# Kernel tuning notes

Hardware: AMD Instinct MI355X
Metric: run time of the kernel (lower is better)

Reference implementation:

```python
import jax, jax.numpy as jnp
import numpy as np

D_MODEL = 1024
N_HEADS = 16
HEAD_DIM = D_MODEL // N_HEADS


def setup_inputs() -> dict:
    key = jax.random.key(0)
    k1, k2, k3 = jax.random.split(key, 3)
    x = jax.random.normal(k1, (4, 2048, D_MODEL), dtype=jnp.float32)
    # torch Linear(d, 3d, bias=False): y = x @ W.T ; store transposed weight [d, 3d]
    scale = 1.0 / np.sqrt(D_MODEL)
    W_qkv = jax.random.normal(k2, (D_MODEL, 3 * D_MODEL), dtype=jnp.float32) * scale
    W_proj = jax.random.normal(k3, (D_MODEL, D_MODEL), dtype=jnp.float32) * scale
    return {"x": x, "W_qkv": W_qkv, "W_proj": W_proj}


def reference(x, W_qkv, W_proj):
    B, T, C = x.shape
    h, d = N_HEADS, HEAD_DIM
    qkv = x @ W_qkv                      # [B,T,3C]
    q, k, v = jnp.split(qkv, 3, axis=-1)
    def split_heads(t):
        return t.reshape(B, T, h, d).transpose(0, 2, 1, 3)  # [B,h,T,d]
    q, k, v = map(split_heads, (q, k, v))
    att = jnp.einsum('bhqd,bhkd->bhqk', q, k) / np.sqrt(d)  # [B,h,T,T]
    causal = jnp.tril(jnp.ones((T, T), dtype=bool))
    att = jnp.where(causal, att, -jnp.inf)
    att = jax.nn.softmax(att, axis=-1)
    # dropout = 0.0 (eval mode): no-op
    y = jnp.einsum('bhqk,bhkd->bhqd', att, v)               # [B,h,T,d]
    y = y.transpose(0, 2, 1, 3).reshape(B, T, C)
    return y @ W_proj
```

## Files before the change

### kernel.cpp

```cpp
#include <hip/hip_runtime.h>

#define T_SEQ 2048
#define D_MODEL 1024
#define NB 4
#define NH 16
#define HD 64

typedef __attribute__((ext_vector_type(8))) __bf16 bf16x8;
typedef __attribute__((ext_vector_type(4))) __bf16 bf16x4;
typedef __attribute__((ext_vector_type(4))) float f32x4;

__device__ __forceinline__ void gload_lds16(const void* g, void* l) {
  __builtin_amdgcn_global_load_lds((const __attribute__((address_space(1))) unsigned int*)g,
                                   (__attribute__((address_space(3))) unsigned int*)l,
                                   16, 0, 0);
}

__device__ __forceinline__ unsigned int pack_bf16_2(float e0, float e1) {
  unsigned short u0 = __builtin_bit_cast(unsigned short, (__bf16)e0);
  unsigned short u1 = __builtin_bit_cast(unsigned short, (__bf16)e1);
  return (unsigned int)u0 | ((unsigned int)u1 << 16);
}

__global__ __launch_bounds__(256) void cvt_bf16_kernel(const float* __restrict__ s,
                                                       __bf16* __restrict__ d, int n) {
  int i = (blockIdx.x * 256 + threadIdx.x) * 8;
  if (i >= n) return;
  float4 a = *(const float4*)(s + i);
  float4 b = *(const float4*)(s + i + 4);
  bf16x8 v;
  v[0] = (__bf16)a.x; v[1] = (__bf16)a.y; v[2] = (__bf16)a.z; v[3] = (__bf16)a.w;
  v[4] = (__bf16)b.x; v[5] = (__bf16)b.y; v[6] = (__bf16)b.z; v[7] = (__bf16)b.w;
  *(bf16x8*)(d + i) = v;
}

__global__ __launch_bounds__(256) void transpose_cvt_kernel(const float* __restrict__ W,
                                                            __bf16* __restrict__ Wt,
                                                            int K, int N) {
  __shared__ float t[32][33];
  int tx = threadIdx.x, ty = threadIdx.y;
  int n0 = blockIdx.x * 32, k0 = blockIdx.y * 32;
#pragma unroll
  for (int r = 0; r < 4; ++r)
    t[ty + r * 8][tx] = W[(size_t)(k0 + ty + r * 8) * N + n0 + tx];
  __syncthreads();
#pragma unroll
  for (int r = 0; r < 4; ++r)
    Wt[(size_t)(n0 + ty + r * 8) * K + k0 + tx] = (__bf16)t[tx][ty + r * 8];
}

__global__ __launch_bounds__(256) void extract_vt_kernel(const __bf16* __restrict__ qkv,
                                                         __bf16* __restrict__ Vt) {
  __shared__ __bf16 t[32][34];
  int tx = threadIdx.x, ty = threadIdx.y;
  int tt = blockIdx.x * 32;
  int dt = blockIdx.y * 32;
  int bh = blockIdx.z;
  int b = bh >> 4, h = bh & 15;
#pragma unroll
  for (int r = 0; r < 4; ++r)
    t[ty + r * 8][tx] = qkv[(size_t)(b * T_SEQ + tt + ty + r * 8) * 3072 + 2048 + h * HD + dt + tx];
  __syncthreads();
#pragma unroll
  for (int r = 0; r < 4; ++r)
    Vt[(size_t)(bh * HD + dt + ty + r * 8) * T_SEQ + tt + tx] = t[tx][ty + r * 8];
}

template <typename OutT>
__global__ __launch_bounds__(256) void gemm_bt(const __bf16* __restrict__ A,
                                               const __bf16* __restrict__ Bt,
                                               OutT* __restrict__ C,
                                               int M, int N, int K) {
  __shared__ __bf16 lA[128 * 64];
  __shared__ __bf16 lB[128 * 64];
  int tid = threadIdx.x;
  int lane = tid & 63, w = tid >> 6;
  int wm = w >> 1, wn = w & 1;
  int bn = blockIdx.x, bm = blockIdx.y;
  f32x4 acc[4][4] = {};
  for (int kt = 0; kt < K; kt += 64) {
#pragma unroll
    for (int it = 0; it < 4; ++it) {
      int o = it * 4096 + tid * 16;
      int row = o >> 7;
      int ss = ((o >> 4) & 7) ^ (row & 7);
      gload_lds16(A + (size_t)(bm * 128 + row) * K + kt + ss * 8, (char*)lA + o);
      gload_lds16(Bt + (size_t)(bn * 128 + row) * K + kt + ss * 8, (char*)lB + o);
    }
    __syncthreads();
    bf16x8 af[4][2], bfv[4][2];
#pragma unroll
    for (int i = 0; i < 4; ++i)
#pragma unroll
      for (int kk = 0; kk < 2; ++kk) {
        int ra = wm * 64 + i * 16 + (lane & 15);
        int sa = ((lane >> 4) + kk * 4) ^ (ra & 7);
        af[i][kk] = *(const bf16x8*)((const char*)lA + ra * 128 + sa * 16);
        int rb = wn * 64 + i * 16 + (lane & 15);
        int sb = ((lane >> 4) + kk * 4) ^ (rb & 7);
        bfv[i][kk] = *(const bf16x8*)((const char*)lB + rb * 128 + sb * 16);
      }
#pragma unroll
    for (int kk = 0; kk < 2; ++kk)
#pragma unroll
      for (int i = 0; i < 4; ++i)
#pragma unroll
        for (int j = 0; j < 4; ++j)
          acc[i][j] = __builtin_amdgcn_mfma_f32_16x16x32_bf16(af[i][kk], bfv[j][kk], acc[i][j], 0, 0, 0);
    __syncthreads();
  }
#pragma unroll
  for (int i = 0; i < 4; ++i)
#pragma unroll
    for (int j = 0; j < 4; ++j)
#pragma unroll
      for (int r = 0; r < 4; ++r) {
        int row = bm * 128 + wm * 64 + i * 16 + (lane >> 4) * 4 + r;
        int col = bn * 128 + wn * 64 + j * 16 + (lane & 15);
        C[(size_t)row * N + col] = (OutT)acc[i][j][r];
      }
}

__global__ __launch_bounds__(256) void attn_kernel(const __bf16* __restrict__ qkv,
                                                   const __bf16* __restrict__ Vt,
                                                   __bf16* __restrict__ Y) {
  __shared__ __bf16 lK[2][64 * 64];
  __shared__ __bf16 lV[2][64 * 64];
  int tid = threadIdx.x, lane = tid & 63, w = tid >> 6;
  int q = lane & 15, g = lane >> 4;

  int l = blockIdx.x;
  int j0 = l >> 3;
  int pair = ((l & 7) << 3) | (j0 >> 4);
  int p = j0 & 15;
  int h = pair & 15;
  int b = pair >> 4;

  const float SCALE = 0.125f * 1.44269504088896f;
  const f32x4 fzero = {0.f, 0.f, 0.f, 0.f};

#pragma unroll 1
  for (int pass = 0; pass < 2; ++pass) {
    int qt = pass ? p : 31 - p;

    const __bf16* qp = qkv + (size_t)(b * T_SEQ + qt * 64 + w * 16 + q) * 3072 + h * HD;
    bf16x8 qf[2];
    qf[0] = *(const bf16x8*)(qp + g * 8);
    qf[1] = *(const bf16x8*)(qp + 32 + g * 8);
#pragma unroll
    for (int kk = 0; kk < 2; ++kk)
#pragma unroll
      for (int jj = 0; jj < 8; ++jj) qf[kk][jj] = (__bf16)((float)qf[kk][jj] * SCALE);

    float m = -INFINITY, lsum = 0.f;
    f32x4 yacc[4];
#pragma unroll
    for (int f = 0; f < 4; ++f) yacc[f] = fzero;

    asm volatile("s_waitcnt vmcnt(0)" ::: "memory");
    __builtin_amdgcn_sched_barrier(0);

    auto STAGE = [&](int kvt, int bi) {
#pragma unroll
      for (int it = 0; it < 2; ++it) {
        int o = it * 4096 + tid * 16;
        int row = o >> 7;
        int ss = ((o >> 4) & 7) ^ (row & 7);
        gload_lds16(qkv + (size_t)(b * T_SEQ + kvt * 64 + row) * 3072 + 1024 + h * HD + ss * 8,
                    (char*)lK[bi] + o);
        gload_lds16(Vt + (size_t)((b * NH + h) * HD + row) * T_SEQ + kvt * 64 + ss * 8,
                    (char*)lV[bi] + o);
      }
    };

    STAGE(0, 0);

#pragma unroll 1
    for (int kvt = 0; kvt <= qt; ++kvt) {
      int cur = kvt & 1;
      if (kvt < qt) {
        STAGE(kvt + 1, cur ^ 1);
        asm volatile("s_waitcnt vmcnt(4)" ::: "memory");
      } else {
        asm volatile("s_waitcnt vmcnt(0)" ::: "memory");
      }
      __builtin_amdgcn_sched_barrier(0);
      __builtin_amdgcn_s_barrier();
      __builtin_amdgcn_sched_barrier(0);

      f32x4 s[4];
#pragma unroll
      for (int f = 0; f < 4; ++f) s[f] = fzero;
      const char* Kbase = (const char*)lK[cur];
      __builtin_amdgcn_s_setprio(1);
#pragma unroll
      for (int kk = 0; kk < 2; ++kk)
#pragma unroll
        for (int f = 0; f < 4; ++f) {
          int rk = f * 16 + q;
          int sk = (g + kk * 4) ^ (rk & 7);
          bf16x8 kf = *(const bf16x8*)(Kbase + rk * 128 + sk * 16);
          s[f] = __builtin_amdgcn_mfma_f32_16x16x32_bf16(kf, qf[kk], s[f], 0, 0, 0);
        }
      __builtin_amdgcn_s_setprio(0);

      if (kvt == qt) {
        int qloc = w * 16 + q;
#pragma unroll
        for (int f = 0; f < 4; ++f)
#pragma unroll
          for (int r = 0; r < 4; ++r)
            if (f * 16 + g * 4 + r > qloc) s[f][r] = -INFINITY;
      }
      float mx = fmaxf(fmaxf(fmaxf(s[0][0], s[0][1]), fmaxf(s[0][2], s[0][3])),
                       fmaxf(fmaxf(s[1][0], s[1][1]), fmaxf(s[1][2], s[1][3])));
      mx = fmaxf(mx, fmaxf(fmaxf(fmaxf(s[2][0], s[2][1]), fmaxf(s[2][2], s[2][3])),
                           fmaxf(fmaxf(s[3][0], s[3][1]), fmaxf(s[3][2], s[3][3]))));
      mx = fmaxf(mx, __shfl_xor(mx, 16, 64));
      mx = fmaxf(mx, __shfl_xor(mx, 32, 64));
      bool grew = mx > m;
      float alpha = 1.0f;
      if (grew) {
        alpha = exp2f(m - mx);
        m = mx;
        lsum *= alpha;
      }
      if (__any(grew)) {
#pragma unroll
        for (int r = 0; r < 4; ++r) {
          float ar = __shfl(alpha, g * 4 + r, 64);
#pragma unroll
          for (int f = 0; f < 4; ++f) yacc[f][r] *= ar;
        }
      }
      float ps = 0.f;
      unsigned int W[4][2];
#pragma unroll
      for (int f = 0; f < 4; ++f)
#pragma unroll
        for (int hh = 0; hh < 2; ++hh) {
          float e0 = exp2f(s[f][2 * hh] - m);
          float e1 = exp2f(s[f][2 * hh + 1] - m);
          ps += e0 + e1;
          W[f][hh] = pack_bf16_2(e0, e1);
        }
      lsum += ps;

      int srcA = ((g & 1) << 5) | q;
      int srcB = srcA + 16;
      bool hisel = (g >= 2);
      bf16x8 pa[2];
#pragma unroll
      for (int kk = 0; kk < 2; ++kk) {
        unsigned int pw[4];
#pragma unroll
        for (int t = 0; t < 4; ++t) {
          int src = (t < 2) ? srcA : srcB;
          unsigned int c0 = (unsigned int)__shfl((int)W[2 * kk][t & 1], src, 64);
          unsigned int c1 = (unsigned int)__shfl((int)W[2 * kk + 1][t & 1], src, 64);
          pw[t] = hisel ? c1 : c0;
        }
        uint4 u = make_uint4(pw[0], pw[1], pw[2], pw[3]);
        pa[kk] = __builtin_bit_cast(bf16x8, u);
      }

      const char* Vbase = (const char*)lV[cur];
      __builtin_amdgcn_s_setprio(1);
#pragma unroll
      for (int kk = 0; kk < 2; ++kk)
#pragma unroll
        for (int f = 0; f < 4; ++f) {
          int rv = f * 16 + q;
          int sv2 = (g + kk * 4) ^ (rv & 7);
          bf16x8 vf = *(const bf16x8*)(Vbase + rv * 128 + sv2 * 16);
          yacc[f] = __builtin_amdgcn_mfma_f32_16x16x32_bf16(pa[kk], vf, yacc[f], 0, 0, 0);
        }
      __builtin_amdgcn_s_setprio(0);

      __builtin_amdgcn_sched_barrier(0);
      asm volatile("s_waitcnt lgkmcnt(0)" ::: "memory");
      __builtin_amdgcn_s_barrier();
      __builtin_amdgcn_sched_barrier(0);
    }

    float ls = lsum;
    ls += __shfl_xor(ls, 16, 64);
    ls += __shfl_xor(ls, 32, 64);
    float linv = 1.0f / ls;
    int qrow = qt * 64 + w * 16 + g * 4;
#pragma unroll
    for (int r = 0; r < 4; ++r) {
      float lr = __shfl(linv, g * 4 + r, 64);
#pragma unroll
      for (int f = 0; f < 4; ++f) {
        Y[(size_t)(b * T_SEQ + qrow + r) * D_MODEL + h * HD + f * 16 + q] =
            (__bf16)(yacc[f][r] * lr);
      }
    }
  }
}

extern "C" void kernel_launch(void* const* d_in, const int* in_sizes, int n_in,
                              void* d_out, int out_size, void* d_ws, size_t ws_size,
                              hipStream_t stream) {
  const float* x = (const float*)d_in[0];
  const float* Wqkv = (const float*)d_in[1];
  const float* Wproj = (const float*)d_in[2];
  float* out = (float*)d_out;
  char* ws = (char*)d_ws;

  __bf16* Xbf     = (__bf16*)(ws);
  __bf16* Wqkv_t  = (__bf16*)(ws + 16777216);
  __bf16* Wproj_t = (__bf16*)(ws + 23068672);
  __bf16* QKV     = (__bf16*)(ws + 25165824);
  __bf16* Vt      = (__bf16*)(ws + 75497472);
  __bf16* Yb      = (__bf16*)(ws + 92274688);

  cvt_bf16_kernel<<<4096, 256, 0, stream>>>(x, Xbf, NB * T_SEQ * D_MODEL);
  transpose_cvt_kernel<<<dim3(96, 32), dim3(32, 8), 0, stream>>>(Wqkv, Wqkv_t, 1024, 3072);
  transpose_cvt_kernel<<<dim3(32, 32), dim3(32, 8), 0, stream>>>(Wproj, Wproj_t, 1024, 1024);
  gemm_bt<__bf16><<<dim3(24, 64), 256, 0, stream>>>(Xbf, Wqkv_t, QKV, 8192, 3072, 1024);
  extract_vt_kernel<<<dim3(64, 2, 64), dim3(32, 8), 0, stream>>>(QKV, Vt);
  attn_kernel<<<1024, 256, 0, stream>>>(QKV, Vt, Yb);
  gemm_bt<float><<<dim3(8, 64), 256, 0, stream>>>(Yb, Wproj_t, out, 8192, 1024, 1024);
}
```

Before: 316.1 us.

## Swizzle GEMM block order, lazy softmax rescale, occupancy hint for attention

The GEMM now remaps the linear block id so groups of consecutive workgroups cover strided tiles, meant to improve L2 reuse across the chiplet-style dispatch. The attention kernel gets a launch-bounds occupancy hint of 4 blocks per CU and a simplified block-to-(batch,head,tile) mapping. The online softmax now rescales only when the running max grows by more than 8 (in log2 units), skipping most rescale work. The trade-off is that exponentials can reach up to 2^8 before the max updates, which keeps fp32 accuracy but puts larger values into the bf16 P operand.

```diff
diff --git a/kernel.cpp b/kernel.cpp
--- a/kernel.cpp
+++ b/kernel.cpp
@@ -76,7 +76,11 @@
   int tid = threadIdx.x;
   int lane = tid & 63, w = tid >> 6;
   int wm = w >> 1, wn = w & 1;
-  int bn = blockIdx.x, bm = blockIdx.y;
+  int nwgx = gridDim.x;
+  int lid = blockIdx.y * nwgx + blockIdx.x;
+  int cpx = (nwgx * gridDim.y) >> 3;
+  int swz = (lid & 7) * cpx + (lid >> 3);
+  int bn = swz % nwgx, bm = swz / nwgx;
   f32x4 acc[4][4] = {};
   for (int kt = 0; kt < K; kt += 64) {
 #pragma unroll
@@ -121,20 +125,18 @@
       }
 }
 
-__global__ __launch_bounds__(256) void attn_kernel(const __bf16* __restrict__ qkv,
-                                                   const __bf16* __restrict__ Vt,
-                                                   __bf16* __restrict__ Y) {
+__global__ __launch_bounds__(256, 4) void attn_kernel(const __bf16* __restrict__ qkv,
+                                                      const __bf16* __restrict__ Vt,
+                                                      __bf16* __restrict__ Y) {
   __shared__ __bf16 lK[2][64 * 64];
   __shared__ __bf16 lV[2][64 * 64];
   int tid = threadIdx.x, lane = tid & 63, w = tid >> 6;
   int q = lane & 15, g = lane >> 4;
 
   int l = blockIdx.x;
-  int j0 = l >> 3;
-  int pair = ((l & 7) << 3) | (j0 >> 4);
-  int p = j0 & 15;
-  int h = pair & 15;
-  int b = pair >> 4;
+  int pairHB = ((l & 7) << 3) | (l >> 7);
+  int p = (l >> 3) & 15;
+  int h = pairHB & 15, b = pairHB >> 4;
 
   const float SCALE = 0.125f * 1.44269504088896f;
   const f32x4 fzero = {0.f, 0.f, 0.f, 0.f};
@@ -212,29 +214,29 @@
           for (int r = 0; r < 4; ++r)
             if (f * 16 + g * 4 + r > qloc) s[f][r] = -INFINITY;
       }
+
       float mx = fmaxf(fmaxf(fmaxf(s[0][0], s[0][1]), fmaxf(s[0][2], s[0][3])),
                        fmaxf(fmaxf(s[1][0], s[1][1]), fmaxf(s[1][2], s[1][3])));
       mx = fmaxf(mx, fmaxf(fmaxf(fmaxf(s[2][0], s[2][1]), fmaxf(s[2][2], s[2][3])),
                            fmaxf(fmaxf(s[3][0], s[3][1]), fmaxf(s[3][2], s[3][3]))));
       mx = fmaxf(mx, __shfl_xor(mx, 16, 64));
       mx = fmaxf(mx, __shfl_xor(mx, 32, 64));
-      bool grew = mx > m;
-      float alpha = 1.0f;
-      if (grew) {
-        alpha = exp2f(m - mx);
-        m = mx;
-        lsum *= alpha;
-      }
-      if (__any(grew)) {
+
+      if (__any(mx - m > 8.0f)) {
+        float mn = fmaxf(m, mx);
+        float al = exp2f(m - mn);
+        m = mn;
+        lsum *= al;
 #pragma unroll
         for (int r = 0; r < 4; ++r) {
-          float ar = __shfl(alpha, g * 4 + r, 64);
+          float ar = __shfl(al, g * 4 + r, 64);
 #pragma unroll
           for (int f = 0; f < 4; ++f) yacc[f][r] *= ar;
         }
       }
+
       float ps = 0.f;
-      unsigned int W[4][2];
+      unsigned int Wd[4][2];
 #pragma unroll
       for (int f = 0; f < 4; ++f)
 #pragma unroll
@@ -242,7 +244,7 @@
           float e0 = exp2f(s[f][2 * hh] - m);
           float e1 = exp2f(s[f][2 * hh + 1] - m);
           ps += e0 + e1;
-          W[f][hh] = pack_bf16_2(e0, e1);
+          Wd[f][hh] = pack_bf16_2(e0, e1);
         }
       lsum += ps;
 
@@ -256,8 +258,8 @@
 #pragma unroll
         for (int t = 0; t < 4; ++t) {
           int src = (t < 2) ? srcA : srcB;
-          unsigned int c0 = (unsigned int)__shfl((int)W[2 * kk][t & 1], src, 64);
-          unsigned int c1 = (unsigned int)__shfl((int)W[2 * kk + 1][t & 1], src, 64);
+          unsigned int c0 = (unsigned int)__shfl((int)Wd[2 * kk][t & 1], src, 64);
+          unsigned int c1 = (unsigned int)__shfl((int)Wd[2 * kk + 1][t & 1], src, 64);
           pw[t] = hisel ? c1 : c0;
         }
         uint4 u = make_uint4(pw[0], pw[1], pw[2], pw[3]);
```

Measured after the change: 277.5 us. -12.2%, faster.
